# Kernel optimization log

Measured on AMD Instinct MI355X. Metric: run time of the kernel, lower is better.

The kernel has to match this reference:

```python
import jax, jax.numpy as jnp
import numpy as np

N_NODES = 100000
N_EDGES = 1600000
NFEAT, NHID, NCLASS = 256, 128, 40


def setup_inputs() -> dict:
    key = jax.random.key(0)
    ks = jax.random.split(key, 10)
    x = jax.random.normal(ks[0], (N_NODES, NFEAT), dtype=jnp.float32)
    edge_row = jnp.sort(jax.random.randint(ks[1], (N_EDGES,), 0, N_NODES, dtype=jnp.int64))
    edge_col = jax.random.randint(ks[2], (N_EDGES,), 0, N_NODES, dtype=jnp.int64)
    edge_val = jax.random.uniform(ks[3], (N_EDGES,), dtype=jnp.float32)
    s = 0.05  # small init scale for numerical stability
    w1 = jax.random.normal(ks[4], (NFEAT, NHID), dtype=jnp.float32) * s
    b1 = jax.random.normal(ks[5], (NHID,), dtype=jnp.float32) * s
    w2 = jax.random.normal(ks[6], (NHID, NHID // 2), dtype=jnp.float32) * s
    b2 = jax.random.normal(ks[7], (NHID // 2,), dtype=jnp.float32) * s
    wl = jax.random.normal(ks[8], (NHID + NHID // 2, NCLASS), dtype=jnp.float32) * s
    bl = jax.random.normal(ks[9], (NCLASS,), dtype=jnp.float32) * s
    return {"x": x, "edge_row": edge_row, "edge_col": edge_col, "edge_val": edge_val,
            "w1": w1, "b1": b1, "w2": w2, "b2": b2, "wl": wl, "bl": bl}


def _gcn_layer(h, w, b, edge_row, edge_col, edge_val, n_nodes):
    # support = h @ W; out = spmm(adj, support) + b  (pygcn GraphConvolution)
    support = h @ w                                   # [N, d_out]
    msg = support[edge_col] * edge_val[:, None]       # gather src + edge weight, [E, d_out]
    agg = jax.ops.segment_sum(msg, edge_row, num_segments=n_nodes)  # scatter-add to dst
    return agg + b


def reference(x, edge_row, edge_col, edge_val, w1, b1, w2, b2, wl, bl):
    n = x.shape[0]
    x1 = jax.nn.relu(_gcn_layer(x, w1, b1, edge_row, edge_col, edge_val, n))
    # dropout is identity in eval mode
    x2 = jax.nn.relu(_gcn_layer(x1, w2, b2, edge_row, edge_col, edge_val, n))
    out = jnp.concatenate([x2, x1], axis=1) @ wl + bl
    return jax.nn.log_softmax(out, axis=-1)
```

## Files before the change

kernel.cpp:

```cpp
#include <hip/hip_runtime.h>
#include <math.h>

#define N_NODES 100000
#define N_EDGES 1600000
#define NFEAT   256
#define NHID    128
#define NHID2   64
#define NCLASS  40
#define NCLS_P  64

typedef __attribute__((ext_vector_type(8))) short bf16x8;
typedef __attribute__((ext_vector_type(4))) float f32x4;
typedef __attribute__((ext_vector_type(2))) float f32x2;

static __device__ inline unsigned short f2bf(float f) {
    union { float f; unsigned u; } v; v.f = f;
    unsigned r = v.u + 0x7FFF + ((v.u >> 16) & 1);
    return (unsigned short)(r >> 16);
}
static __device__ inline unsigned pkbf(float a, float b) {
    return (unsigned)f2bf(a) | ((unsigned)f2bf(b) << 16);
}
static __device__ inline float bfl(unsigned u) {
    union { unsigned u; float f; } v; v.u = u << 16; return v.f;
}
static __device__ inline float bfraw(unsigned u) {
    union { unsigned u; float f; } v; v.u = u; return v.f;
}

#if __has_builtin(__builtin_amdgcn_cvt_pk_fp8_f32) && __has_builtin(__builtin_amdgcn_cvt_pk_f32_fp8)
#define FP8_HW 1
#else
#define FP8_HW 0
static __device__ inline unsigned f2fp8_sw(float f) {
    union { float f; unsigned u; } v; v.f = f;
    unsigned s = (v.u >> 24) & 0x80u;
    int e = (int)((v.u >> 23) & 0xFF) - 120;
    unsigned m = v.u & 0x7FFFFFu;
    if (e < 1) return s;
    unsigned keep = m >> 20, rest = m & 0xFFFFFu;
    keep += (rest > 0x80000u) || (rest == 0x80000u && (keep & 1));
    if (keep == 8) { keep = 0; ++e; }
    if (e > 15) { e = 15; keep = 6; }
    return s | ((unsigned)e << 3) | keep;
}
static __device__ inline float fp8f_sw(unsigned b) {
    unsigned e = (b >> 3) & 0xF;
    union { unsigned u; float f; } v;
    v.u = ((b & 0x80u) << 24) | ((e + 120) << 23) | ((b & 7u) << 20);
    return e ? v.f : 0.f;
}
#endif

static __device__ inline unsigned pack4_fp8(float a, float b, float c, float d) {
#if FP8_HW
    int r = __builtin_amdgcn_cvt_pk_fp8_f32(a, b, 0, false);
    r = __builtin_amdgcn_cvt_pk_fp8_f32(c, d, r, true);
    return (unsigned)r;
#else
    return f2fp8_sw(a) | (f2fp8_sw(b) << 8) | (f2fp8_sw(c) << 16) | (f2fp8_sw(d) << 24);
#endif
}
static __device__ inline void unpack4_fp8(unsigned g, f32x2& lo, f32x2& hi) {
#if FP8_HW
    lo = __builtin_amdgcn_cvt_pk_f32_fp8((int)g, false);
    hi = __builtin_amdgcn_cvt_pk_f32_fp8((int)g, true);
#else
    lo.x = fp8f_sw(g & 0xFF); lo.y = fp8f_sw((g >> 8) & 0xFF);
    hi.x = fp8f_sw((g >> 16) & 0xFF); hi.y = fp8f_sw(g >> 24);
#endif
}

#define PREP_T0 (N_NODES + 1)
#define PREP_T1 (PREP_T0 + NHID * NFEAT)
#define PREP_T2 (PREP_T1 + NHID2 * NHID)
#define PREP_T3 (PREP_T2 + NCLS_P * 192)
#define PREP_T4 (PREP_T3 + N_EDGES)
__global__ void prep(const int* __restrict__ er, int* __restrict__ row_ptr,
                     const float* __restrict__ w1, unsigned short* __restrict__ w1t,
                     const float* __restrict__ w2, unsigned short* __restrict__ w2t,
                     const float* __restrict__ wl, unsigned short* __restrict__ wlt,
                     const int* __restrict__ ec, const float* __restrict__ ev,
                     uint2* __restrict__ meta) {
    int idx = blockIdx.x * blockDim.x + threadIdx.x;
    if (idx < PREP_T0) {
        int lo = 0, hi = N_EDGES;
        while (lo < hi) { int mid = (lo + hi) >> 1; if (er[mid] < idx) lo = mid + 1; else hi = mid; }
        row_ptr[idx] = lo;
    } else if (idx < PREP_T1) {
        int i = idx - PREP_T0;
        int n = i >> 8, k = i & 255;
        w1t[i] = f2bf(w1[k * NHID + n]);
    } else if (idx < PREP_T2) {
        int i = idx - PREP_T1;
        int n = i >> 7, k = i & 127;
        w2t[i] = f2bf(w2[k * NHID2 + n]);
    } else if (idx < PREP_T3) {
        int i = idx - PREP_T2;
        int n = i / 192, k = i - n * 192;
        wlt[i] = (n < NCLASS) ? f2bf(wl[k * NCLASS + n]) : (unsigned short)0;
    } else if (idx < PREP_T4) {
        int i = idx - PREP_T3;
        uint2 m; m.x = (unsigned)ec[i];
        union { float f; unsigned u; } v; v.f = ev[i];
        m.y = v.u;
        meta[i] = m;
    }
}

__global__ __launch_bounds__(256) void conv_fp8(const uint4* __restrict__ sup16,
                                                uint2* __restrict__ sup8, int nw) {
    int i = blockIdx.x * blockDim.x + threadIdx.x;
    if (i >= nw) return;
    uint4 s = sup16[i];
    uint2 r;
    r.x = pack4_fp8(bfl(s.x), bfraw(s.x), bfl(s.y), bfraw(s.y));
    r.y = pack4_fp8(bfl(s.z), bfraw(s.z), bfl(s.w), bfraw(s.w));
    sup8[i] = r;
}

template <int BN, int K, int ABF16, int CBF16>
__global__ __launch_bounds__(512) void gemm_bf16(const void* __restrict__ A,
                                                 const unsigned short* __restrict__ Bt,
                                                 void* __restrict__ C,
                                                 int M, int lda) {
    const int BKP = 40;
    const int NT = K / 32;
    const int WC = (BN == 128) ? 4 : 2;
    const int WR = 8 / WC;
    const int MF = (128 / WR) / 16;
    const int NF = (BN / WC) / 16;
    __shared__ unsigned short As[2][128 * BKP];
    __shared__ unsigned short Bs[2][BN * BKP];

    int tid = threadIdx.x;
    int lane = tid & 63, wid = tid >> 6;
    int wr = wid / WC, wc = wid % WC;
    int row0 = blockIdx.x * 128;

    f32x4 acc[MF][NF];
    #pragma unroll
    for (int i = 0; i < MF; ++i)
        #pragma unroll
        for (int j = 0; j < NF; ++j) acc[i][j] = f32x4{0.f, 0.f, 0.f, 0.f};

    float4 arf[2][2]; uint4 arb[2]; uint4 brg[2];

    auto LOAD = [&](int t, int b) {
        int k0 = t * 32;
        if (ABF16) {
            const unsigned short* Ab = (const unsigned short*)A;
            int m = tid >> 2, k = (tid & 3) * 8;
            int row = row0 + m;
            arb[b] = (row < M) ? *(const uint4*)(Ab + (size_t)row * lda + k0 + k)
                               : uint4{0u, 0u, 0u, 0u};
        } else {
            const float* Af = (const float*)A;
            #pragma unroll
            for (int i = 0; i < 2; ++i) {
                int s = tid + i * 512;
                int m = s >> 3, k = (s & 7) * 4;
                int row = row0 + m;
                arf[b][i] = (row < M) ? *(const float4*)(Af + (size_t)row * lda + k0 + k)
                                      : float4{0.f, 0.f, 0.f, 0.f};
            }
        }
        if (BN == 128 || tid < 256) {
            int n = tid >> 2, k = (tid & 3) * 8;
            brg[b] = *(const uint4*)(Bt + (size_t)n * K + k0 + k);
        }
    };
    auto STORE = [&](int t, int b) {
        int buf = t & 1;
        if (ABF16) {
            int m = tid >> 2, k = (tid & 3) * 8;
            *(uint4*)&As[buf][m * BKP + k] = arb[b];
        } else {
            #pragma unroll
            for (int i = 0; i < 2; ++i) {
                int s = tid + i * 512;
                int m = s >> 3, k = (s & 7) * 4;
                uint2 p; p.x = pkbf(arf[b][i].x, arf[b][i].y); p.y = pkbf(arf[b][i].z, arf[b][i].w);
                *(uint2*)&As[buf][m * BKP + k] = p;
            }
        }
        if (BN == 128 || tid < 256) {
            int n = tid >> 2, k = (tid & 3) * 8;
            *(uint4*)&Bs[buf][n * BKP + k] = brg[b];
        }
    };

    LOAD(0, 0); STORE(0, 0); LOAD(1, 1);
    if (NT > 2) LOAD(2, 0);
    __syncthreads();

    #pragma unroll
    for (int t = 0; t < NT; ++t) {
        int cur = t & 1;
        bf16x8 af[MF], bfr[NF];
        #pragma unroll
        for (int mi = 0; mi < MF; ++mi)
            af[mi] = *(const bf16x8*)&As[cur][(wr * (MF * 16) + mi * 16 + (lane & 15)) * BKP + (lane >> 4) * 8];
        #pragma unroll
        for (int ni = 0; ni < NF; ++ni)
            bfr[ni] = *(const bf16x8*)&Bs[cur][(wc * (NF * 16) + ni * 16 + (lane & 15)) * BKP + (lane >> 4) * 8];
        #pragma unroll
        for (int mi = 0; mi < MF; ++mi)
            #pragma unroll
            for (int ni = 0; ni < NF; ++ni)
                acc[mi][ni] = __builtin_amdgcn_mfma_f32_16x16x32_bf16(af[mi], bfr[ni], acc[mi][ni], 0, 0, 0);
        if (t + 1 < NT) {
            STORE(t + 1, (t + 1) & 1);
            if (t + 3 < NT) LOAD(t + 3, (t + 1) & 1);
            __syncthreads();
        }
    }

    #pragma unroll
    for (int mi = 0; mi < MF; ++mi) {
        int rbase = row0 + wr * (MF * 16) + mi * 16 + ((lane >> 4) << 2);
        #pragma unroll
        for (int ni = 0; ni < NF; ++ni) {
            int col = wc * (NF * 16) + ni * 16 + (lane & 15);
            #pragma unroll
            for (int r = 0; r < 4; ++r) {
                int row = rbase + r;
                if (row < M) {
                    if (CBF16) ((unsigned short*)C)[(size_t)row * BN + col] = f2bf(acc[mi][ni][r]);
                    else       ((float*)C)[(size_t)row * BN + col] = acc[mi][ni][r];
                }
            }
        }
    }
}

__global__ __launch_bounds__(256) void spmm_fp8(const unsigned char* __restrict__ sup8,
                                                const int* __restrict__ row_ptr,
                                                const uint2* __restrict__ meta,
                                                const float* __restrict__ bias,
                                                unsigned short* __restrict__ out,
                                                int out_stride, int n_nodes) {
    __shared__ uint2 mlds[4][64];

    int wave = threadIdx.x >> 6;
    int lane = threadIdx.x & 63;
    int node = blockIdx.x * 4 + wave;
    if (node >= n_nodes) return;

    int sub = lane >> 5, l = lane & 31;
    int e0 = row_ptr[node];
    int cnt = row_ptr[node + 1] - e0;
    unsigned loff = (unsigned)(l << 2);

    f32x2 a0 = {0.f, 0.f}, a1 = {0.f, 0.f};

    for (int o = 0; o < cnt; o += 64) {
        int rem = min(64, cnt - o);
        uint2 m;
        if (lane < rem) m = meta[e0 + o + lane];
        else { m.x = 0u; m.y = 0u; }
        mlds[wave][lane] = m;

        for (int j = 0; j < rem; j += 16) {
            unsigned g[8]; float vv[8];
            #pragma unroll
            for (int t = 0; t < 8; ++t) {
                uint2 cm = mlds[wave][j + 2 * t + sub];
                g[t] = *(const unsigned*)(sup8 + (((size_t)cm.x) << 7) + loff);
                union { unsigned u; float f; } c; c.u = cm.y;
                vv[t] = c.f;
            }
            #pragma unroll
            for (int t = 0; t < 8; ++t) {
                f32x2 lo, hi;
                unpack4_fp8(g[t], lo, hi);
                f32x2 v2 = {vv[t], vv[t]};
                a0 += v2 * lo;
                a1 += v2 * hi;
            }
        }
    }

    a0.x += __shfl_xor(a0.x, 32); a0.y += __shfl_xor(a0.y, 32);
    a1.x += __shfl_xor(a1.x, 32); a1.y += __shfl_xor(a1.y, 32);

    if (lane < 32) {
        float4 bv = *(const float4*)(bias + 4 * l);
        float r0 = a0.x + bv.x, r1 = a0.y + bv.y;
        float r2 = a1.x + bv.z, r3 = a1.y + bv.w;
        r0 = r0 > 0.f ? r0 : 0.f; r1 = r1 > 0.f ? r1 : 0.f;
        r2 = r2 > 0.f ? r2 : 0.f; r3 = r3 > 0.f ? r3 : 0.f;
        uint2 pk; pk.x = pkbf(r0, r1); pk.y = pkbf(r2, r3);
        *(uint2*)(out + (size_t)node * out_stride + 4 * l) = pk;
    }
}

__global__ __launch_bounds__(256) void spmm_bf16_64(const unsigned short* __restrict__ sup,
                                                    const int* __restrict__ row_ptr,
                                                    const uint2* __restrict__ meta,
                                                    const float* __restrict__ bias,
                                                    unsigned short* __restrict__ out,
                                                    int out_stride, int n_nodes) {
    __shared__ uint2 mlds[4][64];

    int wave = threadIdx.x >> 6;
    int lane = threadIdx.x & 63;
    int node = blockIdx.x * 4 + wave;
    if (node >= n_nodes) return;

    int sub = lane >> 4, l = lane & 15;
    int e0 = row_ptr[node];
    int cnt = row_ptr[node + 1] - e0;
    const char* base = (const char*)sup;
    unsigned loff = (unsigned)(l << 3);

    f32x2 a0 = {0.f, 0.f}, a1 = {0.f, 0.f};

    for (int o = 0; o < cnt; o += 64) {
        int rem = min(64, cnt - o);
        uint2 m;
        if (lane < rem) m = meta[e0 + o + lane];
        else { m.x = 0u; m.y = 0u; }
        mlds[wave][lane] = m;

        for (int j = 0; j < rem; j += 32) {
            uint2 g[8]; float vv[8];
            #pragma unroll
            for (int t = 0; t < 8; ++t) {
                uint2 cm = mlds[wave][j + 4 * t + sub];
                unsigned voff = (cm.x << 7) + loff;
                g[t] = *(const uint2*)(base + voff);
                union { unsigned u; float f; } c; c.u = cm.y;
                vv[t] = c.f;
            }
            #pragma unroll
            for (int t = 0; t < 8; ++t) {
                f32x2 v2 = {vv[t], vv[t]};
                f32x2 f0 = {bfl(g[t].x), bfraw(g[t].x)};
                f32x2 f1 = {bfl(g[t].y), bfraw(g[t].y)};
                a0 += v2 * f0;
                a1 += v2 * f1;
            }
        }
    }

    a0.x += __shfl_xor(a0.x, 32); a0.y += __shfl_xor(a0.y, 32);
    a1.x += __shfl_xor(a1.x, 32); a1.y += __shfl_xor(a1.y, 32);
    a0.x += __shfl_xor(a0.x, 16); a0.y += __shfl_xor(a0.y, 16);
    a1.x += __shfl_xor(a1.x, 16); a1.y += __shfl_xor(a1.y, 16);

    if (lane < 16) {
        float4 bv = *(const float4*)(bias + 4 * l);
        float r0 = a0.x + bv.x, r1 = a0.y + bv.y;
        float r2 = a1.x + bv.z, r3 = a1.y + bv.w;
        r0 = r0 > 0.f ? r0 : 0.f; r1 = r1 > 0.f ? r1 : 0.f;
        r2 = r2 > 0.f ? r2 : 0.f; r3 = r3 > 0.f ? r3 : 0.f;
        uint2 pk; pk.x = pkbf(r0, r1); pk.y = pkbf(r2, r3);
        *(uint2*)(out + (size_t)node * out_stride + 4 * l) = pk;
    }
}

__global__ __launch_bounds__(512) void head_fused(const unsigned short* __restrict__ A,
                                                  const unsigned short* __restrict__ Bt,
                                                  const float* __restrict__ bl,
                                                  float* __restrict__ out, int M) {
    const int BKP = 40;
    const int MF = 2, NF = 2;
    __shared__ unsigned short As[2][128 * BKP];
    __shared__ unsigned short Bs[2][64 * BKP];
    __shared__ float L[128][65];
    __shared__ float bls[NCLASS];

    int tid = threadIdx.x;
    int lane = tid & 63, wid = tid >> 6;
    int wr = wid >> 1, wc = wid & 1;
    int row0 = blockIdx.x * 128;
    if (tid < NCLASS) bls[tid] = bl[tid];

    f32x4 acc[MF][NF];
    #pragma unroll
    for (int i = 0; i < MF; ++i)
        #pragma unroll
        for (int j = 0; j < NF; ++j) acc[i][j] = f32x4{0.f, 0.f, 0.f, 0.f};

    uint4 arb, brg;
    auto LOAD = [&](int t) {
        int k0 = t * 32;
        int m = tid >> 2, k = (tid & 3) * 8;
        int row = row0 + m;
        arb = (row < M) ? *(const uint4*)(A + (size_t)row * 192 + k0 + k)
                        : uint4{0u, 0u, 0u, 0u};
        if (tid < 256) brg = *(const uint4*)(Bt + (size_t)m * 192 + k0 + k);
    };
    auto STORE = [&](int b) {
        int m = tid >> 2, k = (tid & 3) * 8;
        *(uint4*)&As[b][m * BKP + k] = arb;
        if (tid < 256) *(uint4*)&Bs[b][m * BKP + k] = brg;
    };

    const int NT = 6;
    LOAD(0); STORE(0);
    __syncthreads();
    #pragma unroll
    for (int t = 0; t < NT; ++t) {
        int cur = t & 1;
        if (t + 1 < NT) LOAD(t + 1);
        bf16x8 af[MF], bfr[NF];
        #pragma unroll
        for (int mi = 0; mi < MF; ++mi)
            af[mi] = *(const bf16x8*)&As[cur][(wr * 32 + mi * 16 + (lane & 15)) * BKP + (lane >> 4) * 8];
        #pragma unroll
        for (int ni = 0; ni < NF; ++ni)
            bfr[ni] = *(const bf16x8*)&Bs[cur][(wc * 32 + ni * 16 + (lane & 15)) * BKP + (lane >> 4) * 8];
        #pragma unroll
        for (int mi = 0; mi < MF; ++mi)
            #pragma unroll
            for (int ni = 0; ni < NF; ++ni)
                acc[mi][ni] = __builtin_amdgcn_mfma_f32_16x16x32_bf16(af[mi], bfr[ni], acc[mi][ni], 0, 0, 0);
        if (t + 1 < NT) {
            STORE(cur ^ 1);
            __syncthreads();
        }
    }

    #pragma unroll
    for (int mi = 0; mi < MF; ++mi) {
        int rt = wr * 32 + mi * 16 + ((lane >> 4) << 2);
        #pragma unroll
        for (int ni = 0; ni < NF; ++ni) {
            int ct = wc * 32 + ni * 16 + (lane & 15);
            #pragma unroll
            for (int r = 0; r < 4; ++r) L[rt + r][ct] = acc[mi][ni][r];
        }
    }
    __syncthreads();

    {
        int r = tid >> 2, h = tid & 3;
        int row = row0 + r;
        if (row < M) {
            float vals[10];
            float m = -1e30f;
            #pragma unroll
            for (int c = 0; c < 10; ++c) {
                float tv = L[r][h * 10 + c] + bls[h * 10 + c];
                vals[c] = tv;
                m = fmaxf(m, tv);
            }
            m = fmaxf(m, __shfl_xor(m, 1));
            m = fmaxf(m, __shfl_xor(m, 2));
            float s = 0.f;
            #pragma unroll
            for (int c = 0; c < 10; ++c) s += __expf(vals[c] - m);
            s += __shfl_xor(s, 1);
            s += __shfl_xor(s, 2);
            float lg = __logf(s);
            float* o = out + (size_t)row * NCLASS + h * 10;
            #pragma unroll
            for (int c = 0; c < 10; ++c) o[c] = vals[c] - m - lg;
        }
    }
}

extern "C" void kernel_launch(void* const* d_in, const int* in_sizes, int n_in,
                              void* d_out, int out_size, void* d_ws, size_t ws_size,
                              hipStream_t stream) {
    const float* x        = (const float*)d_in[0];
    const int*   edge_row = (const int*)d_in[1];
    const int*   edge_col = (const int*)d_in[2];
    const float* edge_val = (const float*)d_in[3];
    const float* w1       = (const float*)d_in[4];
    const float* b1       = (const float*)d_in[5];
    const float* w2       = (const float*)d_in[6];
    const float* b2       = (const float*)d_in[7];
    const float* wl       = (const float*)d_in[8];
    const float* bl       = (const float*)d_in[9];
    float* out = (float*)d_out;
    (void)in_sizes; (void)n_in; (void)out_size; (void)ws_size;

    char* ws = (char*)d_ws;
    size_t off = 0;
    int* row_ptr = (int*)(ws + off);
    off += (((size_t)(N_NODES + 1) * sizeof(int)) + 255) & ~(size_t)255;
    unsigned short* x_cat = (unsigned short*)(ws + off);
    off += (size_t)N_NODES * 192 * sizeof(short);
    unsigned short* sup = (unsigned short*)(ws + off);
    off += (size_t)N_NODES * NHID * sizeof(short);
    unsigned char* sup8 = (unsigned char*)(ws + off);
    off += (size_t)N_NODES * NHID;
    uint2* meta = (uint2*)(ws + off);   off += (size_t)N_EDGES * sizeof(uint2);
    unsigned short* w1t = (unsigned short*)(ws + off); off += (size_t)NHID * NFEAT * sizeof(short);
    unsigned short* w2t = (unsigned short*)(ws + off); off += (size_t)NHID2 * NHID * sizeof(short);
    unsigned short* wlt = (unsigned short*)(ws + off); off += (size_t)NCLS_P * 192 * sizeof(short);

    unsigned short* x1 = x_cat + NHID2;
    unsigned short* x2 = x_cat;

    prep<<<(PREP_T4 + 255) / 256, 256, 0, stream>>>(edge_row, row_ptr, w1, w1t, w2, w2t, wl, wlt,
                                                    edge_col, edge_val, meta);

    int mblocks = (N_NODES + 127) / 128;

    gemm_bf16<NHID, NFEAT, 0, 1><<<dim3(mblocks, 1), 512, 0, stream>>>(x, w1t, sup, N_NODES, NFEAT);
    conv_fp8<<<(N_NODES * NHID / 8 + 255) / 256, 256, 0, stream>>>((const uint4*)sup, (uint2*)sup8,
                                                                   N_NODES * NHID / 8);
    spmm_fp8<<<(N_NODES + 3) / 4, 256, 0, stream>>>(sup8, row_ptr, meta, b1, x1, 192, N_NODES);

    gemm_bf16<NHID2, NHID, 1, 1><<<dim3(mblocks, 1), 512, 0, stream>>>(x1, w2t, sup, N_NODES, 192);
    spmm_bf16_64<<<(N_NODES + 3) / 4, 256, 0, stream>>>(sup, row_ptr, meta, b2, x2, 192, N_NODES);

    head_fused<<<dim3(mblocks, 1), 512, 0, stream>>>(x_cat, wlt, bl, out, N_NODES);
}
```

Before: 163.4 us.

## Fuse FP8 conversion into first GEMM epilogue and load full K tiles at once

The first GEMM now writes FP8 support directly through an LDS-staged epilogue, which removes the separate conv_fp8 kernel and its bf16 intermediate round trip. All three GEMMs (layer 1, layer 2 and head) now load the whole K extent of A and B into dynamic shared memory in one pass and drop the per-K-tile double-buffered pipeline and its per-step barriers. The costs are a large LDS footprint per block (about 135KB for layer 1), which may lower occupancy, and no overlap of global loads with MFMA work. FP8 packing now reads fp32 accumulators directly rather than rounding to bf16 first.

```diff
diff --git a/kernel.cpp b/kernel.cpp
--- a/kernel.cpp
+++ b/kernel.cpp
@@ -108,128 +108,147 @@
     }
 }
 
-__global__ __launch_bounds__(256) void conv_fp8(const uint4* __restrict__ sup16,
-                                                uint2* __restrict__ sup8, int nw) {
-    int i = blockIdx.x * blockDim.x + threadIdx.x;
-    if (i >= nw) return;
-    uint4 s = sup16[i];
-    uint2 r;
-    r.x = pack4_fp8(bfl(s.x), bfraw(s.x), bfl(s.y), bfraw(s.y));
-    r.y = pack4_fp8(bfl(s.z), bfraw(s.z), bfl(s.w), bfraw(s.w));
-    sup8[i] = r;
-}
-
-template <int BN, int K, int ABF16, int CBF16>
-__global__ __launch_bounds__(512) void gemm_bf16(const void* __restrict__ A,
+template <int BN, int K, int ABF16, int CMODE>
+__global__ __launch_bounds__(512) void gemm_full(const void* __restrict__ A,
                                                  const unsigned short* __restrict__ Bt,
                                                  void* __restrict__ C,
-                                                 int M, int lda) {
-    const int BKP = 40;
-    const int NT = K / 32;
-    const int WC = (BN == 128) ? 4 : 2;
-    const int WR = 8 / WC;
-    const int MF = (128 / WR) / 16;
-    const int NF = (BN / WC) / 16;
-    __shared__ unsigned short As[2][128 * BKP];
-    __shared__ unsigned short Bs[2][BN * BKP];
+                                                 int M, int lda, int ldc) {
+    const int S   = K + 8;
+    const int OCT = K / 8;
+    const int WC  = (BN == 128) ? 4 : 2;
+    const int MF  = (BN == 128) ? 4 : 2;
+    const int NF  = 2;
+    const int NT  = K / 32;
+
+    extern __shared__ char smem[];
+    unsigned short* As = (unsigned short*)smem;
+    unsigned short* Bs = As + 128 * S;
 
     int tid = threadIdx.x;
     int lane = tid & 63, wid = tid >> 6;
     int wr = wid / WC, wc = wid % WC;
     int row0 = blockIdx.x * 128;
 
+    if (ABF16) {
+        const unsigned short* Ab = (const unsigned short*)A;
+        const int NI = 128 * OCT / 512;
+        uint4 av[NI];
+        #pragma unroll
+        for (int i = 0; i < NI; ++i) {
+            int s = tid + i * 512;
+            int m = s / OCT, kk = (s - m * OCT) * 8;
+            int row = row0 + m;
+            av[i] = (row < M) ? *(const uint4*)(Ab + (size_t)row * lda + kk)
+                              : uint4{0u, 0u, 0u, 0u};
+        }
+        #pragma unroll
+        for (int i = 0; i < NI; ++i) {
+            int s = tid + i * 512;
+            int m = s / OCT, kk = (s - m * OCT) * 8;
+            *(uint4*)&As[m * S + kk] = av[i];
+        }
+    } else {
+        const float* Af = (const float*)A;
+        const int NI = 128 * (K / 4) / 512;
+        float4 av[NI];
+        #pragma unroll
+        for (int i = 0; i < NI; ++i) {
+            int s = tid + i * 512;
+            int m = s / (K / 4), c = (s - m * (K / 4)) * 4;
+            int row = row0 + m;
+            av[i] = (row < M) ? *(const float4*)(Af + (size_t)row * lda + c)
+                              : float4{0.f, 0.f, 0.f, 0.f};
+        }
+        #pragma unroll
+        for (int i = 0; i < NI; ++i) {
+            int s = tid + i * 512;
+            int m = s / (K / 4), c = (s - m * (K / 4)) * 4;
+            uint2 p; p.x = pkbf(av[i].x, av[i].y); p.y = pkbf(av[i].z, av[i].w);
+            *(uint2*)&As[m * S + c] = p;
+        }
+    }
+    {
+        const int NI = BN * OCT / 512;
+        uint4 bv[NI];
+        #pragma unroll
+        for (int i = 0; i < NI; ++i) {
+            int s = tid + i * 512;
+            int n = s / OCT, kk = (s - n * OCT) * 8;
+            bv[i] = *(const uint4*)(Bt + (size_t)n * K + kk);
+        }
+        #pragma unroll
+        for (int i = 0; i < NI; ++i) {
+            int s = tid + i * 512;
+            int n = s / OCT, kk = (s - n * OCT) * 8;
+            *(uint4*)&Bs[n * S + kk] = bv[i];
+        }
+    }
+    __syncthreads();
+
     f32x4 acc[MF][NF];
     #pragma unroll
     for (int i = 0; i < MF; ++i)
         #pragma unroll
         for (int j = 0; j < NF; ++j) acc[i][j] = f32x4{0.f, 0.f, 0.f, 0.f};
 
-    float4 arf[2][2]; uint4 arb[2]; uint4 brg[2];
-
-    auto LOAD = [&](int t, int b) {
-        int k0 = t * 32;
-        if (ABF16) {
-            const unsigned short* Ab = (const unsigned short*)A;
-            int m = tid >> 2, k = (tid & 3) * 8;
-            int row = row0 + m;
-            arb[b] = (row < M) ? *(const uint4*)(Ab + (size_t)row * lda + k0 + k)
-                               : uint4{0u, 0u, 0u, 0u};
-        } else {
-            const float* Af = (const float*)A;
-            #pragma unroll
-            for (int i = 0; i < 2; ++i) {
-                int s = tid + i * 512;
-                int m = s >> 3, k = (s & 7) * 4;
-                int row = row0 + m;
-                arf[b][i] = (row < M) ? *(const float4*)(Af + (size_t)row * lda + k0 + k)
-                                      : float4{0.f, 0.f, 0.f, 0.f};
-            }
-        }
-        if (BN == 128 || tid < 256) {
-            int n = tid >> 2, k = (tid & 3) * 8;
-            brg[b] = *(const uint4*)(Bt + (size_t)n * K + k0 + k);
-        }
-    };
-    auto STORE = [&](int t, int b) {
-        int buf = t & 1;
-        if (ABF16) {
-            int m = tid >> 2, k = (tid & 3) * 8;
-            *(uint4*)&As[buf][m * BKP + k] = arb[b];
-        } else {
-            #pragma unroll
-            for (int i = 0; i < 2; ++i) {
-                int s = tid + i * 512;
-                int m = s >> 3, k = (s & 7) * 4;
-                uint2 p; p.x = pkbf(arf[b][i].x, arf[b][i].y); p.y = pkbf(arf[b][i].z, arf[b][i].w);
-                *(uint2*)&As[buf][m * BKP + k] = p;
-            }
-        }
-        if (BN == 128 || tid < 256) {
-            int n = tid >> 2, k = (tid & 3) * 8;
-            *(uint4*)&Bs[buf][n * BKP + k] = brg[b];
-        }
-    };
-
-    LOAD(0, 0); STORE(0, 0); LOAD(1, 1);
-    if (NT > 2) LOAD(2, 0);
-    __syncthreads();
-
     #pragma unroll
     for (int t = 0; t < NT; ++t) {
-        int cur = t & 1;
         bf16x8 af[MF], bfr[NF];
         #pragma unroll
         for (int mi = 0; mi < MF; ++mi)
-            af[mi] = *(const bf16x8*)&As[cur][(wr * (MF * 16) + mi * 16 + (lane & 15)) * BKP + (lane >> 4) * 8];
+            af[mi] = *(const bf16x8*)&As[(wr * (MF * 16) + mi * 16 + (lane & 15)) * S + t * 32 + (lane >> 4) * 8];
         #pragma unroll
         for (int ni = 0; ni < NF; ++ni)
-            bfr[ni] = *(const bf16x8*)&Bs[cur][(wc * (NF * 16) + ni * 16 + (lane & 15)) * BKP + (lane >> 4) * 8];
+            bfr[ni] = *(const bf16x8*)&Bs[(wc * (NF * 16) + ni * 16 + (lane & 15)) * S + t * 32 + (lane >> 4) * 8];
         #pragma unroll
         for (int mi = 0; mi < MF; ++mi)
             #pragma unroll
             for (int ni = 0; ni < NF; ++ni)
                 acc[mi][ni] = __builtin_amdgcn_mfma_f32_16x16x32_bf16(af[mi], bfr[ni], acc[mi][ni], 0, 0, 0);
-        if (t + 1 < NT) {
-            STORE(t + 1, (t + 1) & 1);
-            if (t + 3 < NT) LOAD(t + 3, (t + 1) & 1);
-            __syncthreads();
-        }
-    }
-
-    #pragma unroll
-    for (int mi = 0; mi < MF; ++mi) {
-        int rbase = row0 + wr * (MF * 16) + mi * 16 + ((lane >> 4) << 2);
-        #pragma unroll
-        for (int ni = 0; ni < NF; ++ni) {
-            int col = wc * (NF * 16) + ni * 16 + (lane & 15);
-            #pragma unroll
-            for (int r = 0; r < 4; ++r) {
-                int row = rbase + r;
-                if (row < M) {
-                    if (CBF16) ((unsigned short*)C)[(size_t)row * BN + col] = f2bf(acc[mi][ni][r]);
-                    else       ((float*)C)[(size_t)row * BN + col] = acc[mi][ni][r];
+    }
+
+    if (CMODE == 1) {
+        #pragma unroll
+        for (int mi = 0; mi < MF; ++mi) {
+            int rbase = row0 + wr * (MF * 16) + mi * 16 + ((lane >> 4) << 2);
+            #pragma unroll
+            for (int ni = 0; ni < NF; ++ni) {
+                int col = wc * (NF * 16) + ni * 16 + (lane & 15);
+                #pragma unroll
+                for (int r = 0; r < 4; ++r) {
+                    int row = rbase + r;
+                    if (row < M)
+                        ((unsigned short*)C)[(size_t)row * ldc + col] = f2bf(acc[mi][ni][r]);
                 }
             }
+        }
+    } else {
+        __syncthreads();
+        float* Lf = (float*)As;
+        const int LS = 132;
+        #pragma unroll
+        for (int mi = 0; mi < MF; ++mi) {
+            int rt = wr * (MF * 16) + mi * 16 + ((lane >> 4) << 2);
+            #pragma unroll
+            for (int ni = 0; ni < NF; ++ni) {
+                int ct = wc * (NF * 16) + ni * 16 + (lane & 15);
+                #pragma unroll
+                for (int r = 0; r < 4; ++r) Lf[(rt + r) * LS + ct] = acc[mi][ni][r];
+            }
+        }
+        __syncthreads();
+        int rl = tid >> 2, c0 = (tid & 3) * 32;
+        int row = row0 + rl;
+        if (row < M) {
+            unsigned u[8];
+            #pragma unroll
+            for (int q = 0; q < 8; ++q) {
+                f32x4 v = *(const f32x4*)&Lf[rl * LS + c0 + q * 4];
+                u[q] = pack4_fp8(v[0], v[1], v[2], v[3]);
+            }
+            unsigned char* o = (unsigned char*)C + (size_t)row * 128 + c0;
+            *(uint4*)o = uint4{u[0], u[1], u[2], u[3]};
+            *(uint4*)(o + 16) = uint4{u[4], u[5], u[6], u[7]};
         }
     }
 }
@@ -364,12 +383,14 @@
                                                   const unsigned short* __restrict__ Bt,
                                                   const float* __restrict__ bl,
                                                   float* __restrict__ out, int M) {
-    const int BKP = 40;
-    const int MF = 2, NF = 2;
-    __shared__ unsigned short As[2][128 * BKP];
-    __shared__ unsigned short Bs[2][64 * BKP];
-    __shared__ float L[128][65];
-    __shared__ float bls[NCLASS];
+    const int K = 192, S = K + 8, OCT = K / 8;
+    const int MF = 2, NF = 2, NT = 6;
+
+    extern __shared__ char smem[];
+    unsigned short* As = (unsigned short*)smem;
+    unsigned short* Bs = As + 128 * S;
+    float* L  = (float*)(Bs + 64 * S);
+    float* bls = L + 128 * 65;
 
     int tid = threadIdx.x;
     int lane = tid & 63, wid = tid >> 6;
@@ -377,50 +398,60 @@
     int row0 = blockIdx.x * 128;
     if (tid < NCLASS) bls[tid] = bl[tid];
 
+    {
+        uint4 av[6];
+        #pragma unroll
+        for (int i = 0; i < 6; ++i) {
+            int s = tid + i * 512;
+            int m = s / OCT, kk = (s - m * OCT) * 8;
+            int row = row0 + m;
+            av[i] = (row < M) ? *(const uint4*)(A + (size_t)row * 192 + kk)
+                              : uint4{0u, 0u, 0u, 0u};
+        }
+        #pragma unroll
+        for (int i = 0; i < 6; ++i) {
+            int s = tid + i * 512;
+            int m = s / OCT, kk = (s - m * OCT) * 8;
+            *(uint4*)&As[m * S + kk] = av[i];
+        }
+    }
+    {
+        uint4 bv[3];
+        #pragma unroll
+        for (int i = 0; i < 3; ++i) {
+            int s = tid + i * 512;
+            int n = s / OCT, kk = (s - n * OCT) * 8;
+            bv[i] = *(const uint4*)(Bt + (size_t)n * 192 + kk);
+        }
+        #pragma unroll
+        for (int i = 0; i < 3; ++i) {
+            int s = tid + i * 512;
+            int n = s / OCT, kk = (s - n * OCT) * 8;
+            *(uint4*)&Bs[n * S + kk] = bv[i];
+        }
+    }
+    __syncthreads();
+
     f32x4 acc[MF][NF];
     #pragma unroll
     for (int i = 0; i < MF; ++i)
         #pragma unroll
         for (int j = 0; j < NF; ++j) acc[i][j] = f32x4{0.f, 0.f, 0.f, 0.f};
 
-    uint4 arb, brg;
-    auto LOAD = [&](int t) {
-        int k0 = t * 32;
-        int m = tid >> 2, k = (tid & 3) * 8;
-        int row = row0 + m;
-        arb = (row < M) ? *(const uint4*)(A + (size_t)row * 192 + k0 + k)
-                        : uint4{0u, 0u, 0u, 0u};
-        if (tid < 256) brg = *(const uint4*)(Bt + (size_t)m * 192 + k0 + k);
-    };
-    auto STORE = [&](int b) {
-        int m = tid >> 2, k = (tid & 3) * 8;
-        *(uint4*)&As[b][m * BKP + k] = arb;
-        if (tid < 256) *(uint4*)&Bs[b][m * BKP + k] = brg;
-    };
-
-    const int NT = 6;
-    LOAD(0); STORE(0);
-    __syncthreads();
     #pragma unroll
     for (int t = 0; t < NT; ++t) {
-        int cur = t & 1;
-        if (t + 1 < NT) LOAD(t + 1);
         bf16x8 af[MF], bfr[NF];
         #pragma unroll
         for (int mi = 0; mi < MF; ++mi)
-            af[mi] = *(const bf16x8*)&As[cur][(wr * 32 + mi * 16 + (lane & 15)) * BKP + (lane >> 4) * 8];
+            af[mi] = *(const bf16x8*)&As[(wr * 32 + mi * 16 + (lane & 15)) * S + t * 32 + (lane >> 4) * 8];
         #pragma unroll
         for (int ni = 0; ni < NF; ++ni)
-            bfr[ni] = *(const bf16x8*)&Bs[cur][(wc * 32 + ni * 16 + (lane & 15)) * BKP + (lane >> 4) * 8];
+            bfr[ni] = *(const bf16x8*)&Bs[(wc * 32 + ni * 16 + (lane & 15)) * S + t * 32 + (lane >> 4) * 8];
         #pragma unroll
         for (int mi = 0; mi < MF; ++mi)
             #pragma unroll
             for (int ni = 0; ni < NF; ++ni)
                 acc[mi][ni] = __builtin_amdgcn_mfma_f32_16x16x32_bf16(af[mi], bfr[ni], acc[mi][ni], 0, 0, 0);
-        if (t + 1 < NT) {
-            STORE(cur ^ 1);
-            __syncthreads();
-        }
     }
 
     #pragma unroll
@@ -430,7 +461,7 @@
         for (int ni = 0; ni < NF; ++ni) {
             int ct = wc * 32 + ni * 16 + (lane & 15);
             #pragma unroll
-            for (int r = 0; r < 4; ++r) L[rt + r][ct] = acc[mi][ni][r];
+            for (int r = 0; r < 4; ++r) L[(rt + r) * 65 + ct] = acc[mi][ni][r];
         }
     }
     __syncthreads();
@@ -443,7 +474,7 @@
             float m = -1e30f;
             #pragma unroll
             for (int c = 0; c < 10; ++c) {
-                float tv = L[r][h * 10 + c] + bls[h * 10 + c];
+                float tv = L[r * 65 + h * 10 + c] + bls[h * 10 + c];
                 vals[c] = tv;
                 m = fmaxf(m, tv);
             }
@@ -501,13 +532,15 @@
 
     int mblocks = (N_NODES + 127) / 128;
 
-    gemm_bf16<NHID, NFEAT, 0, 1><<<dim3(mblocks, 1), 512, 0, stream>>>(x, w1t, sup, N_NODES, NFEAT);
-    conv_fp8<<<(N_NODES * NHID / 8 + 255) / 256, 256, 0, stream>>>((const uint4*)sup, (uint2*)sup8,
-                                                                   N_NODES * NHID / 8);
+    const int smem1 = (128 + 128) * (NFEAT + 8) * 2;
+    const int smem2 = (128 + 64) * (NHID + 8) * 2;
+    const int smemH = (128 + 64) * (192 + 8) * 2 + 128 * 65 * 4 + NCLASS * 4;
+
+    gemm_full<NHID, NFEAT, 0, 2><<<dim3(mblocks, 1), 512, smem1, stream>>>(x, w1t, sup8, N_NODES, NFEAT, NHID);
     spmm_fp8<<<(N_NODES + 3) / 4, 256, 0, stream>>>(sup8, row_ptr, meta, b1, x1, 192, N_NODES);
 
-    gemm_bf16<NHID2, NHID, 1, 1><<<dim3(mblocks, 1), 512, 0, stream>>>(x1, w2t, sup, N_NODES, 192);
+    gemm_full<NHID2, NHID, 1, 1><<<dim3(mblocks, 1), 512, smem2, stream>>>(x1, w2t, sup, N_NODES, 192, NHID2);
     spmm_bf16_64<<<(N_NODES + 3) / 4, 256, 0, stream>>>(sup, row_ptr, meta, b2, x2, 192, N_NODES);
 
-    head_fused<<<dim3(mblocks, 1), 512, 0, stream>>>(x_cat, wlt, bl, out, N_NODES);
-}
+    head_fused<<<dim3(mblocks, 1), 512, smemH, stream>>>(x_cat, wlt, bl, out, N_NODES);
+}
```

After: 151.1 us. 1.08x faster.
